# Kernel tuning notes

Measured on AMD Instinct MI355X. Metric: run time of the kernel, lower is better.

## Reference

```python
import jax, jax.numpy as jnp
import numpy as np
import math

H = 2048
NH = 16
NKV = 4
HD = H // NH  # 128
N_REP = NH // NKV
EPS = 1e-6


def rms_norm(x, w, eps=1e-6):
    x32 = x.astype(jnp.float32)
    y = x32 * jax.lax.rsqrt(jnp.mean(x32 * x32, axis=-1, keepdims=True) + eps)
    return (y * w.astype(jnp.float32)).astype(x.dtype)


def mha(normed, key_in, val_in, q_w, k_w, v_w, o_w, bias):
    # normed: [b,s,H]; key_in/val_in: [b,n,H]; bias broadcastable to [b,nh,s,n]
    b, s, _ = normed.shape
    n = key_in.shape[1]
    q = (normed @ q_w).reshape(b, s, NH, HD).transpose(0, 2, 1, 3)      # [b,nh,s,d]
    k = (key_in @ k_w).reshape(b, n, NKV, HD).transpose(0, 2, 1, 3)     # [b,nkv,n,d]
    v = (val_in @ v_w).reshape(b, n, NKV, HD).transpose(0, 2, 1, 3)
    k = jnp.repeat(k, N_REP, axis=1)  # GQA expand -> [b,nh,n,d]
    v = jnp.repeat(v, N_REP, axis=1)
    scores = jnp.einsum('bhsd,bhnd->bhsn', q, k) / math.sqrt(HD) + bias
    probs = jax.nn.softmax(scores.astype(jnp.float32), axis=-1).astype(q.dtype)
    out = jnp.einsum('bhsn,bhnd->bhsd', probs, v)
    out = out.transpose(0, 2, 1, 3).reshape(b, s, NH * HD) @ o_w
    return out, probs


def setup_inputs() -> dict:
    key = jax.random.key(0)
    ks = jax.random.split(key, 20)
    B, S, ND, T = 2, 2048, 64, 2048
    w = lambda k, sh: (jax.random.normal(k, sh, dtype=jnp.float32) * 0.02)
    return {
        'hidden_states': jax.random.normal(ks[0], (B, S, H), dtype=jnp.float32),
        'doc_summary_key': jax.random.normal(ks[1], (B, ND, H), dtype=jnp.float32),
        'doc_summary_value': jax.random.normal(ks[2], (B, ND, H), dtype=jnp.float32),
        'doc_summary_mask': jnp.ones((B, ND), dtype=jnp.float32),
        'token_key': jax.random.normal(ks[3], (B, T, H), dtype=jnp.float32),
        'token_value': jax.random.normal(ks[4], (B, T, H), dtype=jnp.float32),
        'token_mask': jnp.ones((B, T), dtype=jnp.float32),
        'cn_w': jnp.ones((H,), dtype=jnp.float32),
        'cq_w': w(ks[5], (H, NH * HD)),
        'ck_w': w(ks[6], (H, NKV * HD)),
        'cv_w': w(ks[7], (H, NKV * HD)),
        'co_w': w(ks[8], (NH * HD, H)),
        'c_gate': jnp.array([-1.0], dtype=jnp.float32),
        'fn_w': jnp.ones((H,), dtype=jnp.float32),
        'fq_w': w(ks[9], (H, NH * HD)),
        'fk_w': w(ks[10], (H, NKV * HD)),
        'fv_w': w(ks[11], (H, NKV * HD)),
        'fo_w': w(ks[12], (NH * HD, H)),
        'f_gate': jnp.array([-1.0], dtype=jnp.float32),
        'doc_token_map': jax.random.randint(ks[13], (B, T), 0, ND, dtype=jnp.int64)
            if jax.config.jax_enable_x64 else jax.random.randint(ks[13], (B, T), 0, ND).astype(jnp.int32),
    }


def reference(hidden_states, doc_summary_key, doc_summary_value, doc_summary_mask,
              token_key, token_value, token_mask,
              cn_w, cq_w, ck_w, cv_w, co_w, c_gate,
              fn_w, fq_w, fk_w, fv_w, fo_w, f_gate,
              doc_token_map):
    # ---- coarse stage: cross-attention over document summaries ----
    normed = rms_norm(hidden_states, cn_w)
    coarse_bias = ((1.0 - doc_summary_mask) * -1e9)[:, None, None, :]  # [b,1,1,nd]
    attn_out, probs = mha(normed, doc_summary_key, doc_summary_value,
                          cq_w, ck_w, cv_w, co_w, coarse_bias)
    doc_scores = probs.mean(axis=(1, 2))  # [b,nd] avg over heads+query positions
    gate_c = jax.nn.sigmoid(c_gate).astype(attn_out.dtype)
    out = hidden_states + gate_c * attn_out

    # ---- fine stage: cross-attention over token KV with log-doc-score bias ----
    log_ds = jnp.log(doc_scores + EPS)
    doc_bias = jnp.take_along_axis(log_ds, doc_token_map, axis=1)  # [b,T]
    pad_bias = (1.0 - token_mask) * -1e9
    fine_bias = (doc_bias + pad_bias)[:, None, None, :]  # [b,1,1,T]
    normed_f = rms_norm(out, fn_w)
    attn_out_f, _ = mha(normed_f, token_key, token_value,
                        fq_w, fk_w, fv_w, fo_w, fine_bias)
    gate_f = jax.nn.sigmoid(f_gate).astype(attn_out_f.dtype)
    final = out + gate_f * attn_out_f
    return final
```

## Files before the change

### kernel.cpp

```cpp
#include <hip/hip_runtime.h>
#include <hip/hip_bf16.h>

typedef unsigned short u16;
typedef unsigned int u32;
typedef __attribute__((ext_vector_type(8))) short bf16x8;
typedef __attribute__((ext_vector_type(4))) float f32x4;

constexpr int NH = 16;
constexpr int H = 2048;
constexpr float SCALE = 0.08838834764831845f;
constexpr float L2E = 1.4426950408889634f;
constexpr float SCALE2 = SCALE * L2E;
constexpr float THR2 = 8.0f * L2E;

__device__ __forceinline__ u16 f2bf(float f) {
    u32 u = __float_as_uint(f);
    u32 r = u + 0x7fffu + ((u >> 16) & 1u);
    return (u16)(r >> 16);
}
__device__ __forceinline__ u32 pack2(float x, float y) {
    return (u32)f2bf(x) | ((u32)f2bf(y) << 16);
}
__device__ __forceinline__ u32 pack2_cvt(float x, float y) {
    __hip_bfloat162 h = __float22bfloat162_rn(float2{x, y});
    return *reinterpret_cast<u32*>(&h);
}

#define GLD_LDS16(gsrc, ldst)                                                  \
    __builtin_amdgcn_global_load_lds(                                          \
        (const __attribute__((address_space(1))) void*)(gsrc),                 \
        (__attribute__((address_space(3))) void*)(ldst), 16, 0, 0)

__global__ __launch_bounds__(256) void cvt_f32_bf16_2(const float* __restrict__ a,
                                                      u16* __restrict__ oa,
                                                      const float* __restrict__ b,
                                                      u16* __restrict__ ob, int n4) {
    int i = blockIdx.x * 256 + threadIdx.x;
    const float* in;
    u16* out;
    if (i < n4) { in = a; out = oa; }
    else if (i < 2 * n4) { i -= n4; in = b; out = ob; }
    else return;
    float4 v = reinterpret_cast<const float4*>(in)[i];
    uint2 o;
    o.x = pack2(v.x, v.y);
    o.y = pack2(v.z, v.w);
    reinterpret_cast<uint2*>(out)[i] = o;
}

__global__ __launch_bounds__(256)
void transpose_cvt4(const float* __restrict__ i0, const float* __restrict__ i1,
                    const float* __restrict__ i2, const float* __restrict__ i3,
                    u16* __restrict__ o0, u16* __restrict__ o1,
                    u16* __restrict__ o2, u16* __restrict__ o3, int K, int N) {
    const float* in = (blockIdx.z == 0) ? i0 : (blockIdx.z == 1) ? i1
                    : (blockIdx.z == 2) ? i2 : i3;
    u16* out = (blockIdx.z == 0) ? o0 : (blockIdx.z == 1) ? o1
             : (blockIdx.z == 2) ? o2 : o3;
    __shared__ u16 tile[32][33];
    int bn = blockIdx.x * 32, bk = blockIdx.y * 32;
    int tx = threadIdx.x & 31, ty = threadIdx.x >> 5;
#pragma unroll
    for (int r = 0; r < 32; r += 8)
        tile[tx][r + ty] = f2bf(in[(size_t)(bk + r + ty) * N + bn + tx]);
    __syncthreads();
#pragma unroll
    for (int r = 0; r < 32; r += 8)
        out[(size_t)(bn + r + ty) * K + bk + tx] = tile[r + ty][tx];
}

__global__ __launch_bounds__(256) void rmsnorm_kernel(const float* __restrict__ x,
                                                      const float* __restrict__ w,
                                                      u16* __restrict__ y) {
    int r = blockIdx.x;
    const float4* xr = reinterpret_cast<const float4*>(x + (size_t)r * H);
    int t = threadIdx.x;
    float4 v0 = xr[t * 2], v1 = xr[t * 2 + 1];
    float ss = v0.x * v0.x + v0.y * v0.y + v0.z * v0.z + v0.w * v0.w
             + v1.x * v1.x + v1.y * v1.y + v1.z * v1.z + v1.w * v1.w;
#pragma unroll
    for (int d = 1; d < 64; d <<= 1) ss += __shfl_xor(ss, d);
    __shared__ float red[4];
    if ((t & 63) == 0) red[t >> 6] = ss;
    __syncthreads();
    float tot = red[0] + red[1] + red[2] + red[3];
    float rs = rsqrtf(tot * (1.0f / H) + 1e-6f);
    const float4* wr = reinterpret_cast<const float4*>(w);
    float4 w0 = wr[t * 2], w1 = wr[t * 2 + 1];
    uint4 o;
    o.x = pack2(v0.x * rs * w0.x, v0.y * rs * w0.y);
    o.y = pack2(v0.z * rs * w0.z, v0.w * rs * w0.w);
    o.z = pack2(v1.x * rs * w1.x, v1.y * rs * w1.y);
    o.w = pack2(v1.z * rs * w1.z, v1.w * rs * w1.w);
    reinterpret_cast<uint4*>(y + (size_t)r * H)[t] = o;
}

template <int MODE, int BN>
__device__ __forceinline__
void gemm_body(const u16* __restrict__ A, const u16* __restrict__ Bt,
               u16* __restrict__ Cb, float* __restrict__ Cf,
               const float* __restrict__ resid, const float* __restrict__ gate_p,
               int N, int K, int brow, int bcol) {
    constexpr int WN = BN / 32;
    constexpr int BWROWS = BN / 4;
    __shared__ u16 As[2][128 * 64];
    __shared__ u16 Bs[2][BN * 64];
    const int t = threadIdx.x;
    const int lane = t & 63, wid = t >> 6;
    const int wm = wid >> 1, wn = wid & 1;
    const int l15 = lane & 15, hi = lane >> 4;
    const int rsw = l15 & 7;

    f32x4 acc[4][WN] = {};
    const int srow = lane >> 3;
    const int sseg = ((lane & 7) ^ srow) * 8;
    const u16* aBase = A + (size_t)(brow + wid * 32 + srow) * K + sseg;
    const u16* bBase = Bt + (size_t)(bcol + wid * BWROWS + srow) * K + sseg;

#define GSTAGE(KT, BF)                                                          \
    do {                                                                        \
        _Pragma("unroll")                                                       \
        for (int u = 0; u < 4; ++u)                                             \
            GLD_LDS16(aBase + (size_t)(u * 8) * K + (KT),                       \
                      &As[BF][(wid * 32 + u * 8) * 64]);                        \
        _Pragma("unroll")                                                       \
        for (int u = 0; u < BWROWS / 8; ++u)                                    \
            GLD_LDS16(bBase + (size_t)(u * 8) * K + (KT),                       \
                      &Bs[BF][(wid * BWROWS + u * 8) * 64]);                    \
    } while (0)

    GSTAGE(0, 0);
    __syncthreads();
    int buf = 0;
    for (int kt = 0; kt < K; kt += 64) {
        if (kt + 64 < K) GSTAGE(kt + 64, buf ^ 1);
        bf16x8 af[4][2], bfr[WN][2];
#pragma unroll
        for (int i = 0; i < 4; ++i) {
            int row = wm * 64 + i * 16 + l15;
#pragma unroll
            for (int ko = 0; ko < 2; ++ko)
                af[i][ko] = *reinterpret_cast<const bf16x8*>(
                    &As[buf][row * 64 + (((ko * 4 + hi) ^ rsw) * 8)]);
        }
#pragma unroll
        for (int j = 0; j < WN; ++j) {
            int row = wn * (BN / 2) + j * 16 + l15;
#pragma unroll
            for (int ko = 0; ko < 2; ++ko)
                bfr[j][ko] = *reinterpret_cast<const bf16x8*>(
                    &Bs[buf][row * 64 + (((ko * 4 + hi) ^ rsw) * 8)]);
        }
#pragma unroll
        for (int ko = 0; ko < 2; ++ko)
#pragma unroll
            for (int i = 0; i < 4; ++i)
#pragma unroll
                for (int j = 0; j < WN; ++j)
                    acc[i][j] = __builtin_amdgcn_mfma_f32_16x16x32_bf16(
                        af[i][ko], bfr[j][ko], acc[i][j], 0, 0, 0);
        __syncthreads();
        buf ^= 1;
    }
#undef GSTAGE

    float g = 0.f;
    if (MODE == 1) g = 1.0f / (1.0f + expf(-gate_p[0]));
    const int r0 = hi * 4, c0 = l15;
#pragma unroll
    for (int i = 0; i < 4; ++i) {
#pragma unroll
        for (int j = 0; j < WN; ++j) {
            int col = bcol + wn * (BN / 2) + j * 16 + c0;
#pragma unroll
            for (int r = 0; r < 4; ++r) {
                int row = brow + wm * 64 + i * 16 + r0 + r;
                float v = acc[i][j][r];
                if (MODE == 0) Cb[(size_t)row * N + col] = f2bf(v);
                else Cf[(size_t)row * N + col] = resid[(size_t)row * N + col] + g * v;
            }
        }
    }
}

template <int MODE, int BN>
__global__ __launch_bounds__(256)
void gemm_tn(const u16* __restrict__ A, const u16* __restrict__ Bt,
             u16* __restrict__ Cb, float* __restrict__ Cf,
             const float* __restrict__ resid, const float* __restrict__ gate_p,
             int M, int N, int K) {
    int nbx = gridDim.x;
    int nwg = nbx * gridDim.y;
    int lin = blockIdx.y * nbx + blockIdx.x;
    if (!(nwg & 7)) { int q = nwg >> 3; lin = (lin & 7) * q + (lin >> 3); }
    gemm_body<MODE, BN>(A, Bt, Cb, Cf, resid, gate_p, N, K,
                        (lin / nbx) * 128, (lin % nbx) * BN);
}

template <int MODE, int BN>
__global__ __launch_bounds__(256)
void gemm_tn_z2(const u16* __restrict__ A0, const u16* __restrict__ B0, u16* __restrict__ C0,
                const u16* __restrict__ A1, const u16* __restrict__ B1, u16* __restrict__ C1,
                int N, int K) {
    const u16* A = blockIdx.z ? A1 : A0;
    const u16* B = blockIdx.z ? B1 : B0;
    u16* C = blockIdx.z ? C1 : C0;
    gemm_body<MODE, BN>(A, B, C, nullptr, nullptr, nullptr, N, K,
                        blockIdx.y * 128, blockIdx.x * BN);
}

__global__ __launch_bounds__(256)
void coarse_attn(const u16* __restrict__ q, const u16* __restrict__ kc,
                 const u16* __restrict__ vc, const float* __restrict__ mask,
                 float* __restrict__ doc_part, u16* __restrict__ attn_c) {
    constexpr int SC = 2048 / 64;
    int bid = blockIdx.x;
    int b = bid / (NH * SC);
    int rem = bid % (NH * SC);
    int h = rem / SC, sc = rem % SC;
    int kv = h >> 2;
    int t = threadIdx.x, lane = t & 63, wid = t >> 6;
    const int l15 = lane & 15, k0 = (lane >> 4) * 8;

    __shared__ u16 Kt[64 * 136];
    __shared__ u16 Vt[128 * 72];
    __shared__ u16 Pt[4][16 * 72];
    __shared__ float p_acc[64];

    {
        int n = t >> 2, s2 = t & 3;
        const u16* src = kc + (size_t)(b * 64 + n) * 512 + kv * 128;
#pragma unroll
        for (int u = 0; u < 4; ++u) {
            int sg = s2 + u * 4;
            *reinterpret_cast<uint4*>(&Kt[n * 136 + sg * 8]) =
                *reinterpret_cast<const uint4*>(src + sg * 8);
        }
    }
    {
        int n = t & 63, dblk = t >> 6;
        const u16* src = vc + (size_t)(b * 64 + n) * 512 + kv * 128 + dblk * 32;
#pragma unroll
        for (int u = 0; u < 4; ++u) {
            u16 tmp[8];
            *reinterpret_cast<uint4*>(tmp) = *reinterpret_cast<const uint4*>(src + u * 8);
#pragma unroll
            for (int e = 0; e < 8; ++e) Vt[(dblk * 32 + u * 8 + e) * 72 + n] = tmp[e];
        }
    }
    if (t < 64) p_acc[t] = 0.f;
    __syncthreads();

    int qrow = sc * 64 + wid * 16 + l15;
    const u16* qsrc = q + (size_t)(b * 2048 + qrow) * 2048 + h * 128;
    bf16x8 af[4];
#pragma unroll
    for (int kk = 0; kk < 4; ++kk)
        af[kk] = *reinterpret_cast<const bf16x8*>(qsrc + kk * 32 + k0);

    f32x4 sc4[4] = {};
#pragma unroll
    for (int kk = 0; kk < 4; ++kk)
#pragma unroll
        for (int j = 0; j < 4; ++j) {
            bf16x8 bfr = *reinterpret_cast<const bf16x8*>(&Kt[(j * 16 + l15) * 136 + kk * 32 + k0]);
            sc4[j] = __builtin_amdgcn_mfma_f32_16x16x32_bf16(af[kk], bfr, sc4[j], 0, 0, 0);
        }

    float s[4][4];
#pragma unroll
    for (int j = 0; j < 4; ++j) {
        float bia = (1.0f - mask[b * 64 + j * 16 + l15]) * (-1e9f * L2E);
#pragma unroll
        for (int r = 0; r < 4; ++r) s[j][r] = sc4[j][r] * SCALE2 + bia;
    }
    float m4[4], l4[4];
#pragma unroll
    for (int r = 0; r < 4; ++r) {
        float m = fmaxf(fmaxf(s[0][r], s[1][r]), fmaxf(s[2][r], s[3][r]));
#pragma unroll
        for (int d = 1; d < 16; d <<= 1) m = fmaxf(m, __shfl_xor(m, d));
        m4[r] = m;
    }
#pragma unroll
    for (int r = 0; r < 4; ++r) {
        float l = 0.f;
#pragma unroll
        for (int j = 0; j < 4; ++j) { s[j][r] = exp2f(s[j][r] - m4[r]); l += s[j][r]; }
#pragma unroll
        for (int d = 1; d < 16; d <<= 1) l += __shfl_xor(l, d);
        l4[r] = l;
    }
#pragma unroll
    for (int j = 0; j < 4; ++j) {
        float cs = 0.f;
#pragma unroll
        for (int r = 0; r < 4; ++r) {
            float pr = s[j][r] / l4[r];
            Pt[wid][((lane >> 4) * 4 + r) * 72 + j * 16 + l15] = f2bf(pr);
            cs += pr;
        }
        cs += __shfl_xor(cs, 16);
        cs += __shfl_xor(cs, 32);
        if (lane < 16) atomicAdd(&p_acc[j * 16 + lane], cs);
    }
    __syncthreads();

    f32x4 o4[8] = {};
#pragma unroll
    for (int kk2 = 0; kk2 < 2; ++kk2) {
        bf16x8 a2 = *reinterpret_cast<const bf16x8*>(&Pt[wid][l15 * 72 + kk2 * 32 + k0]);
#pragma unroll
        for (int j2 = 0; j2 < 8; ++j2) {
            bf16x8 b2 = *reinterpret_cast<const bf16x8*>(&Vt[(j2 * 16 + l15) * 72 + kk2 * 32 + k0]);
            o4[j2] = __builtin_amdgcn_mfma_f32_16x16x32_bf16(a2, b2, o4[j2], 0, 0, 0);
        }
    }
#pragma unroll
    for (int j2 = 0; j2 < 8; ++j2)
#pragma unroll
        for (int r = 0; r < 4; ++r) {
            int row = sc * 64 + wid * 16 + (lane >> 4) * 4 + r;
            attn_c[(size_t)(b * 2048 + row) * 2048 + h * 128 + j2 * 16 + l15] = f2bf(o4[j2][r]);
        }
    if (t < 64) atomicAdd(&doc_part[(blockIdx.x & 7) * 128 + b * 64 + t], p_acc[t]);
}

__global__ __launch_bounds__(256)
void bias_kernel(const float* __restrict__ doc_part, const int* __restrict__ map,
                 const float* __restrict__ tmask, float* __restrict__ bias) {
    __shared__ float lg[128];
    int t = threadIdx.x;
    if (t < 128) {
        float s = 0.f;
#pragma unroll
        for (int i = 0; i < 8; ++i) s += doc_part[i * 128 + t];
        lg[t] = logf(s / 32768.0f + 1e-6f);
    }
    __syncthreads();
    int i = blockIdx.x * 256 + t;
    if (i >= 2 * 2048) return;
    int b = i >> 11;
    bias[i] = (lg[b * 64 + map[i]] + (1.0f - tmask[i]) * -1e9f) * L2E;
}

__global__ __launch_bounds__(256, 2)
void flash_attn(const u16* __restrict__ q, const u16* __restrict__ kf,
                const u16* __restrict__ vT, const float* __restrict__ bias,
                u16* __restrict__ attn_f) {
    int bid = blockIdx.x;
    int b = bid >> 8;
    int rem = bid & 255;
    int h = rem >> 4, sc = rem & 15;
    int kv = h >> 2;
    int t = threadIdx.x, lane = t & 63, wid = t >> 6;
    const int l15 = lane & 15, hi = lane >> 4;
    const int k0 = hi * 8;
    const int rswp = l15 & 7;

    __shared__ u16 Kt[2][64 * 128];
    __shared__ u16 Vt[2][128 * 64];
    __shared__ u16 Pt[4][32 * 64];

    bf16x8 qf4[2][4];
#pragma unroll
    for (int f = 0; f < 2; ++f) {
        int qrow = sc * 128 + wid * 32 + f * 16 + l15;
        const u16* qsrc = q + (size_t)(b * 2048 + qrow) * 2048 + h * 128;
#pragma unroll
        for (int kk = 0; kk < 4; ++kk)
            qf4[f][kk] = *reinterpret_cast<const bf16x8*>(qsrc + kk * 32 + k0);
    }

    const int krl = lane >> 4, kslot = lane & 15;
    const int vrl = lane >> 3, vslot = lane & 7;
    const u16* kbase = kf + (size_t)(b * 2048) * 512 + kv * 128;
    const u16* vbase = vT + (size_t)(kv * 128) * 4096 + b * 2048;
    const float* bbase = bias + b * 2048;

#define STAGE_K(TT, BF)                                                            \
    do {                                                                           \
        _Pragma("unroll")                                                          \
        for (int u = 0; u < 4; ++u) {                                              \
            int row = wid * 16 + u * 4 + krl;                                      \
            const u16* src = kbase + (size_t)((TT) + row) * 512                    \
                             + ((kslot ^ (row & 7)) * 8);                          \
            GLD_LDS16(src, &Kt[BF][(wid * 16 + u * 4) * 128]);                     \
        }                                                                          \
    } while (0)
#define STAGE_V(TT, BF)                                                            \
    do {                                                                           \
        _Pragma("unroll")                                                          \
        for (int u = 0; u < 4; ++u) {                                              \
            int row = wid * 32 + u * 8 + vrl;                                      \
            const u16* src = vbase + (size_t)row * 4096 + (TT)                     \
                             + ((vslot ^ (row & 7)) * 8);                          \
            GLD_LDS16(src, &Vt[BF][(wid * 32 + u * 8) * 64]);                      \
        }                                                                          \
    } while (0)

    float mstate[2] = {-1e30f, -1e30f}, lstate[2] = {0.f, 0.f};
    f32x4 o4[2][8] = {};

    STAGE_K(0, 0);
    STAGE_V(0, 0);
    __syncthreads();
    int par = 0;

    for (int t0 = 0; t0 < 2048; t0 += 64) {
        int t1 = (t0 + 64) & 2047;
        STAGE_K(t1, par ^ 1);
        STAGE_V(t1, par ^ 1);

        f32x4 st0[4] = {}, st1[4] = {};
        __builtin_amdgcn_s_setprio(1);
#pragma unroll
        for (int kk = 0; kk < 4; ++kk)
#pragma unroll
            for (int kb = 0; kb < 4; ++kb) {
                int row = kb * 16 + l15;
                bf16x8 kfrag = *reinterpret_cast<const bf16x8*>(
                    &Kt[par][row * 128 + (((kk * 4 + hi) ^ (row & 7)) * 8)]);
                st0[kb] = __builtin_amdgcn_mfma_f32_16x16x32_bf16(kfrag, qf4[0][kk], st0[kb], 0, 0, 0);
                st1[kb] = __builtin_amdgcn_mfma_f32_16x16x32_bf16(kfrag, qf4[1][kk], st1[kb], 0, 0, 0);
            }
        __builtin_amdgcn_s_setprio(0);

        float p[2][4][4];
        float pmax[2] = {-1e30f, -1e30f};
#pragma unroll
        for (int kb = 0; kb < 4; ++kb) {
            float4 b4 = *reinterpret_cast<const float4*>(bbase + t0 + kb * 16 + hi * 4);
            float bb[4] = {b4.x, b4.y, b4.z, b4.w};
#pragma unroll
            for (int r = 0; r < 4; ++r) {
                float v0 = st0[kb][r] * SCALE2 + bb[r];
                float v1 = st1[kb][r] * SCALE2 + bb[r];
                p[0][kb][r] = v0;
                p[1][kb][r] = v1;
                pmax[0] = fmaxf(pmax[0], v0);
                pmax[1] = fmaxf(pmax[1], v1);
            }
        }
#pragma unroll
        for (int f = 0; f < 2; ++f) {
            pmax[f] = fmaxf(pmax[f], __shfl_xor(pmax[f], 16));
            pmax[f] = fmaxf(pmax[f], __shfl_xor(pmax[f], 32));
        }

        bool need = (pmax[0] > mstate[0] + THR2) || (pmax[1] > mstate[1] + THR2);
        if (__any(need)) {
#pragma unroll
            for (int f = 0; f < 2; ++f) {
                float mnew = fmaxf(mstate[f], pmax[f]);
                float sco = exp2f(mstate[f] - mnew);
                float sco_out[4];
#pragma unroll
                for (int r = 0; r < 4; ++r) sco_out[r] = __shfl(sco, hi * 4 + r);
#pragma unroll
                for (int j2 = 0; j2 < 8; ++j2)
#pragma unroll
                    for (int r = 0; r < 4; ++r) o4[f][j2][r] *= sco_out[r];
                lstate[f] *= sco;
                mstate[f] = mnew;
            }
        }

#pragma unroll
        for (int f = 0; f < 2; ++f) {
            float lt = 0.f;
#pragma unroll
            for (int kb = 0; kb < 4; ++kb)
#pragma unroll
                for (int r = 0; r < 4; ++r) {
                    p[f][kb][r] = exp2f(p[f][kb][r] - mstate[f]);
                    lt += p[f][kb][r];
                }
            lt += __shfl_xor(lt, 16);
            lt += __shfl_xor(lt, 32);
            lstate[f] += lt;
        }

#pragma unroll
        for (int f = 0; f < 2; ++f)
#pragma unroll
            for (int kb = 0; kb < 4; ++kb) {
                uint2 w;
                w.x = pack2_cvt(p[f][kb][0], p[f][kb][1]);
                w.y = pack2_cvt(p[f][kb][2], p[f][kb][3]);
                int idx = (f * 16 + l15) * 64
                        + (((kb * 2 + (hi >> 1)) ^ rswp) * 8) + (hi & 1) * 4;
                *reinterpret_cast<uint2*>(&Pt[wid][idx]) = w;
            }

        __builtin_amdgcn_s_setprio(1);
#pragma unroll
        for (int kc2 = 0; kc2 < 2; ++kc2) {
            bf16x8 pa0 = *reinterpret_cast<const bf16x8*>(
                &Pt[wid][l15 * 64 + (((kc2 * 4 + hi) ^ rswp) * 8)]);
            bf16x8 pa1 = *reinterpret_cast<const bf16x8*>(
                &Pt[wid][(16 + l15) * 64 + (((kc2 * 4 + hi) ^ rswp) * 8)]);
#pragma unroll
            for (int j2 = 0; j2 < 8; ++j2) {
                int d = j2 * 16 + l15;
                bf16x8 vb = *reinterpret_cast<const bf16x8*>(
                    &Vt[par][d * 64 + (((kc2 * 4 + hi) ^ (d & 7)) * 8)]);
                o4[0][j2] = __builtin_amdgcn_mfma_f32_16x16x32_bf16(pa0, vb, o4[0][j2], 0, 0, 0);
                o4[1][j2] = __builtin_amdgcn_mfma_f32_16x16x32_bf16(pa1, vb, o4[1][j2], 0, 0, 0);
            }
        }
        __builtin_amdgcn_s_setprio(0);
        __syncthreads();
        par ^= 1;
    }
#undef STAGE_K
#undef STAGE_V

#pragma unroll
    for (int f = 0; f < 2; ++f) {
        float linv[4];
#pragma unroll
        for (int r = 0; r < 4; ++r) linv[r] = 1.0f / __shfl(lstate[f], hi * 4 + r);
#pragma unroll
        for (int j2 = 0; j2 < 8; ++j2)
#pragma unroll
            for (int r = 0; r < 4; ++r) {
                int row = sc * 128 + wid * 32 + f * 16 + hi * 4 + r;
                attn_f[(size_t)(b * 2048 + row) * 2048 + h * 128 + j2 * 16 + l15] =
                    f2bf(o4[f][j2][r] * linv[r]);
            }
    }
}

extern "C" void kernel_launch(void* const* d_in, const int* in_sizes, int n_in,
                              void* d_out, int out_size, void* d_ws, size_t ws_size,
                              hipStream_t stream) {
    const float* hidden = (const float*)d_in[0];
    const float* dsk    = (const float*)d_in[1];
    const float* dsv    = (const float*)d_in[2];
    const float* dsmask = (const float*)d_in[3];
    const float* tk     = (const float*)d_in[4];
    const float* tv     = (const float*)d_in[5];
    const float* tmask  = (const float*)d_in[6];
    const float* cn_w   = (const float*)d_in[7];
    const float* cq_w   = (const float*)d_in[8];
    const float* ck_w   = (const float*)d_in[9];
    const float* cv_w   = (const float*)d_in[10];
    const float* co_w   = (const float*)d_in[11];
    const float* c_gate = (const float*)d_in[12];
    const float* fn_w   = (const float*)d_in[13];
    const float* fq_w   = (const float*)d_in[14];
    const float* fk_w   = (const float*)d_in[15];
    const float* fv_w   = (const float*)d_in[16];
    const float* fo_w   = (const float*)d_in[17];
    const float* f_gate = (const float*)d_in[18];
    const int*   map    = (const int*)d_in[19];
    float* out_f = (float*)d_out;

    char* ws = (char*)d_ws;
    size_t off = 0;
    auto alloc = [&](size_t bytes) {
        char* p = ws + off;
        off += (bytes + 255) & ~(size_t)255;
        return p;
    };
    u16*  normA = (u16*)alloc(4096ULL * 2048 * 2);
    u16*  qbuf  = (u16*)alloc(4096ULL * 2048 * 2);
    u16*  kc    = (u16*)alloc(128ULL * 512 * 2);
    u16*  vc    = (u16*)alloc(128ULL * 512 * 2);
    u16*  dskb  = (u16*)alloc(128ULL * 2048 * 2);
    u16*  dsvb  = (u16*)alloc(128ULL * 2048 * 2);
    u16*  kfb   = (u16*)alloc(4096ULL * 512 * 2);
    u16*  vTb   = (u16*)alloc(512ULL * 4096 * 2);
    u16*  tkb   = (u16*)alloc(4096ULL * 2048 * 2);
    u16*  tvb   = (u16*)alloc(4096ULL * 2048 * 2);
    u16*  cqT   = (u16*)alloc(2048ULL * 2048 * 2);
    u16*  ckT   = (u16*)alloc(512ULL * 2048 * 2);
    u16*  cvT   = (u16*)alloc(512ULL * 2048 * 2);
    u16*  coT   = (u16*)alloc(2048ULL * 2048 * 2);
    u16*  fqT   = (u16*)alloc(2048ULL * 2048 * 2);
    u16*  fkT   = (u16*)alloc(512ULL * 2048 * 2);
    u16*  fvT   = (u16*)alloc(512ULL * 2048 * 2);
    u16*  foT   = (u16*)alloc(2048ULL * 2048 * 2);
    float* doc_part = (float*)alloc(8 * 128 * 4);
    float* biasb    = (float*)alloc(4096 * 4);

    hipMemsetAsync(doc_part, 0, 8 * 128 * 4, stream);

    transpose_cvt4<<<dim3(64, 64, 4), 256, 0, stream>>>(cq_w, co_w, fq_w, fo_w,
                                                        cqT, coT, fqT, foT, 2048, 2048);
    transpose_cvt4<<<dim3(16, 64, 4), 256, 0, stream>>>(ck_w, cv_w, fk_w, fv_w,
                                                        ckT, cvT, fkT, fvT, 2048, 512);

    cvt_f32_bf16_2<<<(2 * 128 * 2048 / 4 + 255) / 256, 256, 0, stream>>>(
        dsk, dskb, dsv, dsvb, 128 * 2048 / 4);
    cvt_f32_bf16_2<<<(2 * 4096 * 2048 / 4 + 255) / 256, 256, 0, stream>>>(
        tk, tkb, tv, tvb, 4096 * 2048 / 4);
    rmsnorm_kernel<<<4096, 256, 0, stream>>>(hidden, cn_w, normA);

    gemm_tn<0, 128><<<dim3(16, 32), 256, 0, stream>>>(normA, cqT, qbuf, nullptr, nullptr, nullptr, 4096, 2048, 2048);
    gemm_tn_z2<0, 64><<<dim3(8, 1, 2), 256, 0, stream>>>(dskb, ckT, kc, dsvb, cvT, vc, 512, 2048);

    coarse_attn<<<1024, 256, 0, stream>>>(qbuf, kc, vc, dsmask, doc_part, normA);
    bias_kernel<<<16, 256, 0, stream>>>(doc_part, map, tmask, biasb);

    gemm_tn<1, 128><<<dim3(16, 32), 256, 0, stream>>>(normA, coT, nullptr, out_f, hidden, c_gate, 4096, 2048, 2048);

    rmsnorm_kernel<<<4096, 256, 0, stream>>>(out_f, fn_w, qbuf);
    gemm_tn<0, 128><<<dim3(16, 32), 256, 0, stream>>>(qbuf, fqT, normA, nullptr, nullptr, nullptr, 4096, 2048, 2048);
    gemm_tn<0, 64><<<dim3(8, 32), 256, 0, stream>>>(tkb, fkT, kfb, nullptr, nullptr, nullptr, 4096, 512, 2048);
    gemm_tn<0, 64><<<dim3(64, 4), 256, 0, stream>>>(fvT, tvb, vTb, nullptr, nullptr, nullptr, 512, 4096, 2048);

    flash_attn<<<512, 256, 0, stream>>>(normA, kfb, vTb, biasb, qbuf);

    gemm_tn<1, 128><<<dim3(16, 32), 256, 0, stream>>>(qbuf, foT, nullptr, out_f, out_f, f_gate, 4096, 2048, 2048);
}
```

Measured before the change: 452.0 us.

## Add 256x128-tile triple-buffered GEMM for the four square projections

Introduces a new GEMM kernel with 512 threads, 256x128 output tiles, a three-stage LDS pipeline using direct global-to-LDS loads, and an XOR-swizzled layout. It replaces the 128x128 gemm_tn for the Q and output projections in both stages. Larger tiles raise data reuse per global load and deeper buffering hides memory latency. In exchange it uses much more LDS (about 144KB), allowing one block per CU, and launches 256 blocks, which on a 256-CU part leaves no room for load balancing. The workspace buffer order is also shuffled.

```diff
diff --git a/kernel.cpp b/kernel.cpp
--- a/kernel.cpp
+++ b/kernel.cpp
@@ -207,6 +207,116 @@
     u16* C = blockIdx.z ? C1 : C0;
     gemm_body<MODE, BN>(A, B, C, nullptr, nullptr, nullptr, N, K,
                         blockIdx.y * 128, blockIdx.x * BN);
+}
+
+template <int MODE>
+__global__ __launch_bounds__(512, 1)
+void gemm_big(const u16* __restrict__ A, const u16* __restrict__ Bt,
+              u16* __restrict__ Cb, float* __restrict__ Cf,
+              const float* __restrict__ resid, const float* __restrict__ gate_p,
+              int M, int N, int K) {
+    int nbx = gridDim.x;
+    int nwg = nbx * gridDim.y;
+    int lin = blockIdx.y * nbx + blockIdx.x;
+    if (!(nwg & 7)) { int q = nwg >> 3; lin = (lin & 7) * q + (lin >> 3); }
+    const int brow = (lin / nbx) * 256, bcol = (lin % nbx) * 128;
+
+    __shared__ u16 As[3][256 * 64];
+    __shared__ u16 Bs[3][128 * 64];
+    const int t = threadIdx.x;
+    const int lane = t & 63, wid = t >> 6;
+    const int wm = wid >> 1, wn = wid & 1;
+    const int l15 = lane & 15, hi = lane >> 4;
+    const int rsw = l15 & 7;
+    const int srow = lane >> 3, sslot = lane & 7;
+    const int sseg = (sslot ^ srow) * 8;
+
+    const u16* aBase = A + (size_t)(brow + wid * 32 + srow) * K + sseg;
+    const u16* bBase = Bt + (size_t)(bcol + wid * 16 + srow) * K + sseg;
+
+#define BSTAGE(KT, BF)                                                          \
+    do {                                                                        \
+        _Pragma("unroll")                                                       \
+        for (int u = 0; u < 4; ++u)                                             \
+            GLD_LDS16(aBase + (size_t)(u * 8) * K + (KT),                       \
+                      &As[BF][(wid * 32 + u * 8) * 64]);                        \
+        _Pragma("unroll")                                                       \
+        for (int u = 0; u < 2; ++u)                                             \
+            GLD_LDS16(bBase + (size_t)(u * 8) * K + (KT),                       \
+                      &Bs[BF][(wid * 16 + u * 8) * 64]);                        \
+    } while (0)
+
+    f32x4 acc[4][4] = {};
+    const int nt = K >> 6;
+
+    BSTAGE(0, 0);
+    BSTAGE(64, 1);
+    BSTAGE(128, 2);
+    asm volatile("s_waitcnt vmcnt(12)" ::: "memory");
+    __builtin_amdgcn_sched_barrier(0);
+    asm volatile("s_barrier" ::: "memory");
+
+    int bufc = 0;
+#pragma unroll 1
+    for (int it = 0; it < nt; ++it) {
+        const u16* as = &As[bufc][0];
+        const u16* bs = &Bs[bufc][0];
+        bf16x8 af[4][2], bfr[4][2];
+#pragma unroll
+        for (int i = 0; i < 4; ++i) {
+            int row = wm * 64 + i * 16 + l15;
+#pragma unroll
+            for (int ko = 0; ko < 2; ++ko)
+                af[i][ko] = *reinterpret_cast<const bf16x8*>(
+                    &as[row * 64 + (((ko * 4 + hi) ^ rsw) * 8)]);
+        }
+#pragma unroll
+        for (int j = 0; j < 4; ++j) {
+            int row = wn * 64 + j * 16 + l15;
+#pragma unroll
+            for (int ko = 0; ko < 2; ++ko)
+                bfr[j][ko] = *reinterpret_cast<const bf16x8*>(
+                    &bs[row * 64 + (((ko * 4 + hi) ^ rsw) * 8)]);
+        }
+        __builtin_amdgcn_s_setprio(1);
+#pragma unroll
+        for (int ko = 0; ko < 2; ++ko)
+#pragma unroll
+            for (int i = 0; i < 4; ++i)
+#pragma unroll
+                for (int j = 0; j < 4; ++j)
+                    acc[i][j] = __builtin_amdgcn_mfma_f32_16x16x32_bf16(
+                        af[i][ko], bfr[j][ko], acc[i][j], 0, 0, 0);
+        __builtin_amdgcn_s_setprio(0);
+
+        asm volatile("s_barrier" ::: "memory");
+        if (it + 3 < nt) BSTAGE((it + 3) * 64, bufc);
+        if (it < nt - 3)       asm volatile("s_waitcnt vmcnt(12)" ::: "memory");
+        else if (it == nt - 3) asm volatile("s_waitcnt vmcnt(6)" ::: "memory");
+        else if (it == nt - 2) asm volatile("s_waitcnt vmcnt(0)" ::: "memory");
+        __builtin_amdgcn_sched_barrier(0);
+        asm volatile("s_barrier" ::: "memory");
+        bufc = (bufc == 2) ? 0 : bufc + 1;
+    }
+#undef BSTAGE
+
+    float g = 0.f;
+    if (MODE == 1) g = 1.0f / (1.0f + expf(-gate_p[0]));
+    const int r0 = hi * 4, c0 = l15;
+#pragma unroll
+    for (int i = 0; i < 4; ++i) {
+#pragma unroll
+        for (int j = 0; j < 4; ++j) {
+            int col = bcol + wn * 64 + j * 16 + c0;
+#pragma unroll
+            for (int r = 0; r < 4; ++r) {
+                int row = brow + wm * 64 + i * 16 + r0 + r;
+                float v = acc[i][j][r];
+                if (MODE == 0) Cb[(size_t)row * N + col] = f2bf(v);
+                else Cf[(size_t)row * N + col] = resid[(size_t)row * N + col] + g * v;
+            }
+        }
+    }
 }
 
 __global__ __launch_bounds__(256)
@@ -568,12 +678,12 @@
     u16*  qbuf  = (u16*)alloc(4096ULL * 2048 * 2);
     u16*  kc    = (u16*)alloc(128ULL * 512 * 2);
     u16*  vc    = (u16*)alloc(128ULL * 512 * 2);
-    u16*  dskb  = (u16*)alloc(128ULL * 2048 * 2);
-    u16*  dsvb  = (u16*)alloc(128ULL * 2048 * 2);
     u16*  kfb   = (u16*)alloc(4096ULL * 512 * 2);
     u16*  vTb   = (u16*)alloc(512ULL * 4096 * 2);
     u16*  tkb   = (u16*)alloc(4096ULL * 2048 * 2);
     u16*  tvb   = (u16*)alloc(4096ULL * 2048 * 2);
+    u16*  dskb  = (u16*)alloc(128ULL * 2048 * 2);
+    u16*  dsvb  = (u16*)alloc(128ULL * 2048 * 2);
     u16*  cqT   = (u16*)alloc(2048ULL * 2048 * 2);
     u16*  ckT   = (u16*)alloc(512ULL * 2048 * 2);
     u16*  cvT   = (u16*)alloc(512ULL * 2048 * 2);
@@ -598,20 +708,20 @@
         tk, tkb, tv, tvb, 4096 * 2048 / 4);
     rmsnorm_kernel<<<4096, 256, 0, stream>>>(hidden, cn_w, normA);
 
-    gemm_tn<0, 128><<<dim3(16, 32), 256, 0, stream>>>(normA, cqT, qbuf, nullptr, nullptr, nullptr, 4096, 2048, 2048);
+    gemm_big<0><<<dim3(16, 16), 512, 0, stream>>>(normA, cqT, qbuf, nullptr, nullptr, nullptr, 4096, 2048, 2048);
     gemm_tn_z2<0, 64><<<dim3(8, 1, 2), 256, 0, stream>>>(dskb, ckT, kc, dsvb, cvT, vc, 512, 2048);
 
     coarse_attn<<<1024, 256, 0, stream>>>(qbuf, kc, vc, dsmask, doc_part, normA);
     bias_kernel<<<16, 256, 0, stream>>>(doc_part, map, tmask, biasb);
 
-    gemm_tn<1, 128><<<dim3(16, 32), 256, 0, stream>>>(normA, coT, nullptr, out_f, hidden, c_gate, 4096, 2048, 2048);
+    gemm_big<1><<<dim3(16, 16), 512, 0, stream>>>(normA, coT, nullptr, out_f, hidden, c_gate, 4096, 2048, 2048);
 
     rmsnorm_kernel<<<4096, 256, 0, stream>>>(out_f, fn_w, qbuf);
-    gemm_tn<0, 128><<<dim3(16, 32), 256, 0, stream>>>(qbuf, fqT, normA, nullptr, nullptr, nullptr, 4096, 2048, 2048);
+    gemm_big<0><<<dim3(16, 16), 512, 0, stream>>>(qbuf, fqT, normA, nullptr, nullptr, nullptr, 4096, 2048, 2048);
     gemm_tn<0, 64><<<dim3(8, 32), 256, 0, stream>>>(tkb, fkT, kfb, nullptr, nullptr, nullptr, 4096, 512, 2048);
     gemm_tn<0, 64><<<dim3(64, 4), 256, 0, stream>>>(fvT, tvb, vTb, nullptr, nullptr, nullptr, 512, 4096, 2048);
 
     flash_attn<<<512, 256, 0, stream>>>(normA, kfb, vTb, biasb, qbuf);
 
-    gemm_tn<1, 128><<<dim3(16, 32), 256, 0, stream>>>(qbuf, foT, nullptr, out_f, out_f, f_gate, 4096, 2048, 2048);
-}
+    gemm_big<1><<<dim3(16, 16), 512, 0, stream>>>(qbuf, foT, nullptr, out_f, out_f, f_gate, 4096, 2048, 2048);
+}
```

Result: slower. 475.7 us (+5.2%).
